# Optimization experiments

Measured on AMD Instinct MI355X. Metric: run time of the kernel, lower is better.

## Reference

```python
import jax, jax.numpy as jnp
import numpy as np

GAMMA = 2.0

def _bce_with_logits(x, y):
    # stable: max(x,0) - x*y + log(1+exp(-|x|)) == logaddexp(0,x) - x*y
    return jnp.logaddexp(0.0, x) - x * y

def setup_inputs() -> dict:
    key = jax.random.key(0)
    k1, k2, k3 = jax.random.split(key, 3)
    B = 4_000_000
    logit = jax.random.normal(k1, (B, 7), dtype=jnp.float32)
    label = jax.random.randint(k2, (B,), 0, 2, dtype=jnp.int32)
    repr_mask = jax.random.randint(k3, (B, 7), 0, 2, dtype=jnp.int32)
    return {"logit": logit, "label": label, "repr_mask": repr_mask}

def reference(logit, label, repr_mask):
    B = logit.shape[0]
    logit = logit.reshape(B, -1)                     # [B,7]
    lab = label.astype(logit.dtype)[:, None]         # [B,1], broadcasts like repeat(1,7)
    bce = _bce_with_logits(logit, lab)               # [B,7]
    focal = (1.0 - jnp.exp(-bce)) ** GAMMA * bce
    bce_neg = _bce_with_logits(-logit, 1.0 - lab)
    focal_neg = (1.0 - jnp.exp(-bce_neg)) ** GAMMA * bce_neg
    m = repr_mask.astype(logit.dtype)                # 1 on repr indices
    pos = jnp.sum(focal * m, axis=1)                 # sum over repr_num[i]
    neg = jnp.sum(focal_neg * (1.0 - m), axis=1)     # sum over not_repr
    is_neg_label = (label == 0)
    loss = pos + jnp.where(is_neg_label, neg, jnp.zeros_like(neg))
    return loss
```

## Files before the change

kernel.cpp:

```cpp
#include <hip/hip_runtime.h>


#define TPB 256

__device__ __forceinline__ void focal_both(float x, float& f0, float& f1) {
    float a  = fabsf(x);
    float e  = __expf(-a);
    float r  = __builtin_amdgcn_rcpf(1.0f + e);
    float q  = e * r;
    float Lg = __logf(1.0f + e);
    float tr = q * q * Lg;
    float tq = r * r * (a + Lg);
    bool xpos = (x >= 0.0f);
    f1 = xpos ? tr : tq;
    f0 = xpos ? tq : tr;
}

__global__ __launch_bounds__(TPB, 4) void focal_loss_kernel(
    const float* __restrict__ logit,
    const int*   __restrict__ label,
    const int*   __restrict__ repr_mask,
    float*       __restrict__ out,
    int B)
{
    __shared__ float4 stage[4][448];

    const int tid  = threadIdx.x;
    const int L    = tid & 63;
    const int w    = tid >> 6;
    const int wc   = blockIdx.x * 4 + w;
    const long R0  = (long)wc * 256;

    float4* wbuf = stage[w];

    if (R0 + 256 <= B) {
        const uint4* lg4 = reinterpret_cast<const uint4*>(logit)     + (size_t)wc * 448;
        const uint4* mk4 = reinterpret_cast<const uint4*>(repr_mask) + (size_t)wc * 448;

        uint4 lg[7], mk[7];
#pragma unroll
        for (int k = 0; k < 7; ++k) lg[k] = lg4[k * 64 + L];
#pragma unroll
        for (int k = 0; k < 7; ++k) mk[k] = mk4[k * 64 + L];
        int4 lab4 = reinterpret_cast<const int4*>(label)[(size_t)wc * 64 + L];

        int mu = (4 * L) % 7;
#pragma unroll
        for (int k = 0; k < 7; ++k) {
            float4 xf = *reinterpret_cast<float4*>(&lg[k]);
            float xs[4] = { xf.x, xf.y, xf.z, xf.w };
            unsigned ms[4] = { mk[k].x, mk[k].y, mk[k].z, mk[k].w };

            float A0 = 0.f, A1 = 0.f, B0 = 0.f, B1 = 0.f;
#pragma unroll
            for (int j = 0; j < 4; ++j) {
                float f0, f1;
                focal_both(xs[j], f0, f1);
                float fm = ms[j] ? f1 : 0.0f;
                bool toB = (mu + j) >= 7;
                A0 += toB ? 0.0f : f0;
                B0 += toB ? f0   : 0.0f;
                A1 += toB ? 0.0f : fm;
                B1 += toB ? fm   : 0.0f;
            }
            wbuf[k * 64 + L] = make_float4(A0, A1, B0, B1);
            mu += 4; if (mu >= 7) mu -= 7;
        }

        float4 u0 = wbuf[L * 7 + 0];
        float4 u1 = wbuf[L * 7 + 1];
        float4 u2 = wbuf[L * 7 + 2];
        float4 u3 = wbuf[L * 7 + 3];
        float4 u4 = wbuf[L * 7 + 4];
        float4 u5 = wbuf[L * 7 + 5];
        float4 u6 = wbuf[L * 7 + 6];

        float t0_0 = u0.x + u1.x;
        float t1_0 = u0.y + u1.y;
        float t0_1 = u1.z + u2.x + u3.x;
        float t1_1 = u1.w + u2.y + u3.y;
        float t0_2 = u3.z + u4.x + u5.x;
        float t1_2 = u3.w + u4.y + u5.y;
        float t0_3 = u5.z + u6.x;
        float t1_3 = u5.w + u6.y;

        float4 res;
        res.x = (lab4.x != 0) ? t1_0 : t0_0;
        res.y = (lab4.y != 0) ? t1_1 : t0_1;
        res.z = (lab4.z != 0) ? t1_2 : t0_2;
        res.w = (lab4.w != 0) ? t1_3 : t0_3;
        reinterpret_cast<float4*>(out)[(size_t)wc * 64 + L] = res;
    } else if (R0 < B) {
        long r4 = R0 / 4 + L;
        long Q  = B >> 2;
        if (r4 < Q) {
            float res[4];
#pragma unroll
            for (int r = 0; r < 4; ++r) {
                long row = r4 * 4 + r;
                bool yy = (label[row] != 0);
                float tot = 0.f, ms = 0.f;
                for (int c = 0; c < 7; ++c) {
                    float f0, f1;
                    focal_both(logit[(size_t)row * 7 + c], f0, f1);
                    tot += f0;
                    ms  += repr_mask[(size_t)row * 7 + c] ? f1 : 0.f;
                }
                res[r] = yy ? ms : tot;
            }
            reinterpret_cast<float4*>(out)[r4] =
                make_float4(res[0], res[1], res[2], res[3]);
        }
    }

    if ((B & 3) && blockIdx.x == 0 && tid == 0) {
        for (long row = (long)(B >> 2) * 4; row < B; ++row) {
            bool yy = (label[row] != 0);
            float tot = 0.f, ms = 0.f;
            for (int c = 0; c < 7; ++c) {
                float f0, f1;
                focal_both(logit[(size_t)row * 7 + c], f0, f1);
                tot += f0;
                ms  += repr_mask[(size_t)row * 7 + c] ? f1 : 0.f;
            }
            out[row] = yy ? ms : tot;
        }
    }
}

extern "C" void kernel_launch(void* const* d_in, const int* in_sizes, int n_in,
                              void* d_out, int out_size, void* d_ws, size_t ws_size,
                              hipStream_t stream) {
    const float* logit     = (const float*)d_in[0];
    const int*   label     = (const int*)d_in[1];
    const int*   repr_mask = (const int*)d_in[2];
    float*       out       = (float*)d_out;

    int B = in_sizes[1];
    long chunks = ((long)B + 255) / 256;
    int blocks = (int)((chunks + 3) / 4);
    if (blocks < 1) blocks = 1;

    focal_loss_kernel<<<blocks, TPB, 0, stream>>>(logit, label, repr_mask, out, B);
}
```

Baseline: 45.28 us.

## Shrink LDS staging and software-pipeline loads to raise occupancy

Global loads for the 7 logit/mask chunks are no longer issued all up front. Each iteration now prefetches only the next chunk, which cuts live registers, and the launch-bound occupancy hint rises from 4 to 8. LDS staging shrinks from float4 per chunk to a float2 per chunk plus a compact array that holds only the boundary-spill partial sums. The intent is more waves in flight and less LDS per block for this memory-bound kernel. The cost is fewer outstanding loads per wave and extra index arithmetic.

```diff
diff --git a/kernel.cpp b/kernel.cpp
--- a/kernel.cpp
+++ b/kernel.cpp
@@ -16,40 +16,47 @@
     f0 = xpos ? tq : tr;
 }
 
-__global__ __launch_bounds__(TPB, 4) void focal_loss_kernel(
+__global__ __launch_bounds__(TPB, 8) void focal_loss_kernel(
     const float* __restrict__ logit,
     const int*   __restrict__ label,
     const int*   __restrict__ repr_mask,
     float*       __restrict__ out,
     int B)
 {
-    __shared__ float4 stage[4][448];
+    __shared__ float2 sA[4][448];
+    __shared__ float2 sB[4][192];
 
-    const int tid  = threadIdx.x;
-    const int L    = tid & 63;
-    const int w    = tid >> 6;
-    const int wc   = blockIdx.x * 4 + w;
-    const long R0  = (long)wc * 256;
+    const int tid = threadIdx.x;
+    const int L   = tid & 63;
+    const int w   = tid >> 6;
+    const int wc  = blockIdx.x * 4 + w;
+    const long R0 = (long)wc * 256;
 
-    float4* wbuf = stage[w];
+    float2* A  = sA[w];
+    float2* Bc = sB[w];
 
     if (R0 + 256 <= B) {
         const uint4* lg4 = reinterpret_cast<const uint4*>(logit)     + (size_t)wc * 448;
         const uint4* mk4 = reinterpret_cast<const uint4*>(repr_mask) + (size_t)wc * 448;
-
-        uint4 lg[7], mk[7];
-#pragma unroll
-        for (int k = 0; k < 7; ++k) lg[k] = lg4[k * 64 + L];
-#pragma unroll
-        for (int k = 0; k < 7; ++k) mk[k] = mk4[k * 64 + L];
         int4 lab4 = reinterpret_cast<const int4*>(label)[(size_t)wc * 64 + L];
 
-        int mu = (4 * L) % 7;
+        int m  = (L * 9363) >> 16;
+        int r0 = L - 7 * m;
+        int t4 = 4 * r0;
+        int mu = t4 - 7 * ((t4 * 9363) >> 16);
+
+        uint4 lgc = lg4[L];
+        uint4 mkc = mk4[L];
 #pragma unroll
         for (int k = 0; k < 7; ++k) {
-            float4 xf = *reinterpret_cast<float4*>(&lg[k]);
-            float xs[4] = { xf.x, xf.y, xf.z, xf.w };
-            unsigned ms[4] = { mk[k].x, mk[k].y, mk[k].z, mk[k].w };
+            uint4 lgn, mkn;
+            if (k < 6) {
+                lgn = lg4[(k + 1) * 64 + L];
+                mkn = mk4[(k + 1) * 64 + L];
+            }
+            float4 xf = *reinterpret_cast<float4*>(&lgc);
+            float    xs[4] = { xf.x, xf.y, xf.z, xf.w };
+            unsigned ms[4] = { mkc.x, mkc.y, mkc.z, mkc.w };
 
             float A0 = 0.f, A1 = 0.f, B0 = 0.f, B1 = 0.f;
 #pragma unroll
@@ -63,26 +70,30 @@
                 A1 += toB ? 0.0f : fm;
                 B1 += toB ? fm   : 0.0f;
             }
-            wbuf[k * 64 + L] = make_float4(A0, A1, B0, B1);
+            A[k * 64 + L] = make_float2(A0, A1);
+            if (mu >= 4)
+                Bc[3 * m + (mu - 4)] = make_float2(B0, B1);
+
+            m += (mu == 3) ? 10 : 9;
             mu += 4; if (mu >= 7) mu -= 7;
+            lgc = lgn; mkc = mkn;
         }
 
-        float4 u0 = wbuf[L * 7 + 0];
-        float4 u1 = wbuf[L * 7 + 1];
-        float4 u2 = wbuf[L * 7 + 2];
-        float4 u3 = wbuf[L * 7 + 3];
-        float4 u4 = wbuf[L * 7 + 4];
-        float4 u5 = wbuf[L * 7 + 5];
-        float4 u6 = wbuf[L * 7 + 6];
+        float2 a0 = A[L * 7 + 0];
+        float2 a1 = A[L * 7 + 1];
+        float2 a2 = A[L * 7 + 2];
+        float2 a3 = A[L * 7 + 3];
+        float2 a4 = A[L * 7 + 4];
+        float2 a5 = A[L * 7 + 5];
+        float2 a6 = A[L * 7 + 6];
+        float2 b0 = Bc[L * 3 + 0];
+        float2 b1 = Bc[L * 3 + 1];
+        float2 b2 = Bc[L * 3 + 2];
 
-        float t0_0 = u0.x + u1.x;
-        float t1_0 = u0.y + u1.y;
-        float t0_1 = u1.z + u2.x + u3.x;
-        float t1_1 = u1.w + u2.y + u3.y;
-        float t0_2 = u3.z + u4.x + u5.x;
-        float t1_2 = u3.w + u4.y + u5.y;
-        float t0_3 = u5.z + u6.x;
-        float t1_3 = u5.w + u6.y;
+        float t0_0 = a0.x + a1.x;             float t1_0 = a0.y + a1.y;
+        float t0_1 = b0.x + a2.x + a3.x;      float t1_1 = b0.y + a2.y + a3.y;
+        float t0_2 = b1.x + a4.x + a5.x;      float t1_2 = b1.y + a4.y + a5.y;
+        float t0_3 = b2.x + a6.x;             float t1_3 = b2.y + a6.y;
 
         float4 res;
         res.x = (lab4.x != 0) ? t1_0 : t0_0;
@@ -96,8 +107,8 @@
         if (r4 < Q) {
             float res[4];
 #pragma unroll
-            for (int r = 0; r < 4; ++r) {
-                long row = r4 * 4 + r;
+            for (int rr = 0; rr < 4; ++rr) {
+                long row = r4 * 4 + rr;
                 bool yy = (label[row] != 0);
                 float tot = 0.f, ms = 0.f;
                 for (int c = 0; c < 7; ++c) {
@@ -106,7 +117,7 @@
                     tot += f0;
                     ms  += repr_mask[(size_t)row * 7 + c] ? f1 : 0.f;
                 }
-                res[r] = yy ? ms : tot;
+                res[rr] = yy ? ms : tot;
             }
             reinterpret_cast<float4*>(out)[r4] =
                 make_float4(res[0], res[1], res[2], res[3]);
```

Result: faster. 44.11 us (-2.6%).
